# Kernel optimization log

Measured on AMD Instinct MI355X. Metric: run time of the kernel, lower is better.

## Reference

```python
import jax, jax.numpy as jnp
import numpy as np

N, D, H = 4096, 256, 8
NEG = -4294967295.0  # -2**32 + 1, as in masked_fill


def _layernorm(x, g, b, eps=1e-5):
    mu = jnp.mean(x, axis=-1, keepdims=True)
    var = jnp.var(x, axis=-1, keepdims=True)
    return (x - mu) * jax.lax.rsqrt(var + eps) * g + b


def setup_inputs() -> dict:
    key = jax.random.key(0)
    ks = jax.random.split(key, 12)
    s = 0.02
    return {
        "x": jax.random.normal(ks[0], (N, D), jnp.float32),
        "mask_idx": jax.random.randint(ks[1], (N,), 0, 2, jnp.int32),
        "spatial": jax.random.normal(ks[2], (N, N), jnp.float32),
        "edge": jax.random.normal(ks[3], (N, N), jnp.float32),
        "ln1_g": jnp.ones((D,), jnp.float32),
        "ln1_b": jnp.zeros((D,), jnp.float32),
        "Wq": jax.random.normal(ks[4], (H, D, D), jnp.float32) * s,
        "bq": jnp.zeros((H, D), jnp.float32),
        "Wk": jax.random.normal(ks[5], (H, D, D), jnp.float32) * s,
        "bk": jnp.zeros((H, D), jnp.float32),
        "Wv": jax.random.normal(ks[6], (H, D, D), jnp.float32) * s,
        "bv": jnp.zeros((H, D), jnp.float32),
        "Wo": jax.random.normal(ks[7], (D, H * D), jnp.float32) * s,
        "bo": jnp.zeros((D,), jnp.float32),
        "ln2_g": jnp.ones((D,), jnp.float32),
        "ln2_b": jnp.zeros((D,), jnp.float32),
        "Wff": jax.random.normal(ks[8], (D, D), jnp.float32) * s,
        "bff": jnp.zeros((D,), jnp.float32),
    }


def reference(x, mask_idx, spatial, edge, ln1_g, ln1_b, Wq, bq, Wk, bk, Wv, bv,
              Wo, bo, ln2_g, ln2_b, Wff, bff):
    x_ln = _layernorm(x, ln1_g, ln1_b)
    # per-head projections, torch Linear: y = x W^T + b ; q,k,v: [H, N, D]
    q = jnp.einsum('nd,hed->hne', x_ln, Wq) + bq[:, None, :]
    k = jnp.einsum('nd,hed->hne', x_ln, Wk) + bk[:, None, :]
    v = jnp.einsum('nd,hed->hne', x_ln, Wv) + bv[:, None, :]
    scale = 1.0 / jnp.sqrt(jnp.float32(D))  # dim_q ** 0.5
    a = jnp.einsum('hne,hme->hnm', q, k) * scale  # [H, N, N]
    a = a + spatial[None] + edge[None]
    mask0 = (mask_idx[:, None] * mask_idx[None, :]) == 0  # [N, N]
    a = jnp.where(mask0[None], jnp.float32(NEG), a)
    p = jax.nn.softmax(a, axis=-1)
    p = jnp.where(mask0[None], 0.0, p)
    heads = jnp.einsum('hnm,hme->hne', p, v)  # [H, N, D]
    cat = jnp.transpose(heads, (1, 0, 2)).reshape(N, H * D)
    x_out = cat @ Wo.T + bo + x
    x_attn = _layernorm(x_out, ln2_g, ln2_b) @ Wff.T + bff + x_out
    return x_attn
```

## Files before the change

### kernel.cpp

```cpp
#include <hip/hip_runtime.h>
#include <hip/hip_bf16.h>
#include <hip/hip_fp16.h>
#include <string.h>

typedef unsigned short u16;
typedef __attribute__((ext_vector_type(8))) short short8;
typedef __attribute__((ext_vector_type(4))) float floatx4;
typedef __attribute__((ext_vector_type(16))) float floatx16;

#define N_TOK 4096
#define D_DIM 256
#define H_HEAD 8

__device__ __forceinline__ u16 f2b(float f){
  __hip_bfloat16 h = __float2bfloat16(f);
  return *reinterpret_cast<u16*>(&h);
}
__device__ __forceinline__ float b2f(u16 u){
  union { unsigned u; float f; } c; c.u = ((unsigned)u) << 16; return c.f;
}
__device__ __forceinline__ float h2f(u16 u){
  __half h; *reinterpret_cast<u16*>(&h) = u; return __half2float(h);
}
__device__ __forceinline__ u16 f2h(float f){
  __half h = __float2half(f); return *reinterpret_cast<u16*>(&h);
}
__device__ __forceinline__ unsigned pk2bf(float a, float b){
  __hip_bfloat162 h = __float22bfloat162_rn(make_float2(a, b));
  return *reinterpret_cast<unsigned*>(&h);
}

__device__ __forceinline__ void glds16(const void* g, void* l){
  __builtin_amdgcn_global_load_lds(
      (const __attribute__((address_space(1))) unsigned int*)g,
      (__attribute__((address_space(3))) unsigned int*)l, 16, 0, 0);
}

__global__ void fused_prep(const float* __restrict__ Wq, const float* __restrict__ Wk,
                           const float* __restrict__ Wv, const float* __restrict__ Wo,
                           const float* __restrict__ Wff,
                           const float* __restrict__ bq, const float* __restrict__ bk,
                           const float* __restrict__ bv,
                           u16* __restrict__ wqkv, u16* __restrict__ wo_b,
                           u16* __restrict__ wff_b, float* __restrict__ bqkv){
  int bid = blockIdx.x;
  if (bid == 1056){
    int t = threadIdx.x;
    for (int j = 0; j < 24; ++j){
      int idx = t + j*256;
      float v;
      if (idx < 2048) v = bq[idx];
      else if (idx < 4096) v = bk[idx - 2048];
      else v = bv[idx - 4096];
      bqkv[idx] = v;
    }
    return;
  }
  const float* src; u16* dst; int base;
  if      (bid < 256) { src = Wq;  dst = wqkv;            base = bid; }
  else if (bid < 512) { src = Wk;  dst = wqkv + 524288;   base = bid - 256; }
  else if (bid < 768) { src = Wv;  dst = wqkv + 1048576;  base = bid - 512; }
  else if (bid < 1024){ src = Wo;  dst = wo_b;            base = bid - 768; }
  else                { src = Wff; dst = wff_b;           base = bid - 1024; }
  int i = (base*256 + threadIdx.x)*8;
  float4 a = *(const float4*)(src + i);
  float4 b = *(const float4*)(src + i + 4);
  u16 u[8] = {f2b(a.x),f2b(a.y),f2b(a.z),f2b(a.w),f2b(b.x),f2b(b.y),f2b(b.z),f2b(b.w)};
  *(short8*)(dst + i) = *(short8*)u;
}

__global__ void ln_kernel(const float* __restrict__ x, const float* __restrict__ g,
                          const float* __restrict__ b, u16* __restrict__ out){
  const int row = blockIdx.x;
  const int t = threadIdx.x;
  float v = x[(size_t)row*D_DIM + t];
  float s = v, ss = v*v;
  #pragma unroll
  for (int off = 32; off > 0; off >>= 1){
    s  += __shfl_down(s,  off);
    ss += __shfl_down(ss, off);
  }
  __shared__ float ls[4], lss[4];
  const int w = t >> 6, lane = t & 63;
  if (lane == 0){ ls[w] = s; lss[w] = ss; }
  __syncthreads();
  if (t == 0){
    float S  = ls[0]+ls[1]+ls[2]+ls[3];
    float SS = lss[0]+lss[1]+lss[2]+lss[3];
    float mu = S * (1.0f/D_DIM);
    float var = SS * (1.0f/D_DIM) - mu*mu;
    ls[0] = mu; lss[0] = rsqrtf(var + 1e-5f);
  }
  __syncthreads();
  float mu = ls[0], rs = lss[0];
  out[(size_t)row*D_DIM + t] = f2b((v - mu)*rs*g[t] + b[t]);
}

__global__ void ln_sum(const float* __restrict__ p0, const float* __restrict__ p1,
                       const float* __restrict__ bo, const float* __restrict__ x,
                       const float* __restrict__ g, const float* __restrict__ b,
                       float* __restrict__ xout, u16* __restrict__ xln2){
  const int row = blockIdx.x;
  const int t = threadIdx.x;
  const size_t idx = (size_t)row*D_DIM + t;
  float v = p0[idx] + p1[idx] + bo[t] + x[idx];
  float s = v, ss = v*v;
  #pragma unroll
  for (int off = 32; off > 0; off >>= 1){
    s  += __shfl_down(s,  off);
    ss += __shfl_down(ss, off);
  }
  __shared__ float ls[4], lss[4];
  const int w = t >> 6, lane = t & 63;
  if (lane == 0){ ls[w] = s; lss[w] = ss; }
  __syncthreads();
  if (t == 0){
    float S  = ls[0]+ls[1]+ls[2]+ls[3];
    float SS = lss[0]+lss[1]+lss[2]+lss[3];
    float mu = S * (1.0f/D_DIM);
    float var = SS * (1.0f/D_DIM) - mu*mu;
    ls[0] = mu; lss[0] = rsqrtf(var + 1e-5f);
  }
  __syncthreads();
  float mu = ls[0], rs = lss[0];
  xout[idx] = v;
  xln2[idx] = f2b((v - mu)*rs*g[t] + b[t]);
}

__global__ void make_biasW(const float* __restrict__ sp, const float* __restrict__ ed,
                           const int* __restrict__ mask, u16* __restrict__ out){
  __shared__ u16 bh[32][64];
  const int tg = blockIdx.x, q32 = blockIdx.y;
  const int t = threadIdx.x;
  const float L2E = 1.4426950408889634f;
  const u16 NINF = 0xFC00;
  {
    int ql = t>>3, kc = (t&7)*8;
    size_t off = (size_t)(q32*32 + ql)*N_TOK + tg*64 + kc;
    float4 s0 = *(const float4*)(sp + off);
    float4 s1 = *(const float4*)(sp + off + 4);
    float4 e0 = *(const float4*)(ed + off);
    float4 e1 = *(const float4*)(ed + off + 4);
    int mr = mask[q32*32 + ql];
    int4 m0 = *(const int4*)(mask + tg*64 + kc);
    int4 m1 = *(const int4*)(mask + tg*64 + kc + 4);
    bh[ql][kc+0] = (mr*m0.x)==0 ? NINF : f2h((s0.x+e0.x)*L2E);
    bh[ql][kc+1] = (mr*m0.y)==0 ? NINF : f2h((s0.y+e0.y)*L2E);
    bh[ql][kc+2] = (mr*m0.z)==0 ? NINF : f2h((s0.z+e0.z)*L2E);
    bh[ql][kc+3] = (mr*m0.w)==0 ? NINF : f2h((s0.w+e0.w)*L2E);
    bh[ql][kc+4] = (mr*m1.x)==0 ? NINF : f2h((s1.x+e1.x)*L2E);
    bh[ql][kc+5] = (mr*m1.y)==0 ? NINF : f2h((s1.y+e1.y)*L2E);
    bh[ql][kc+6] = (mr*m1.z)==0 ? NINF : f2h((s1.z+e1.z)*L2E);
    bh[ql][kc+7] = (mr*m1.w)==0 ? NINF : f2h((s1.w+e1.w)*L2E);
  }
  __syncthreads();
  int lane2 = t>>2, j0 = (t&3)*8;
  u16 tmp[8];
  #pragma unroll
  for (int jj = 0; jj < 8; ++jj){
    int j = j0 + jj;
    int nb = j>>4, reg = j&15;
    int kvl = nb*32 + (reg&3) + 8*(reg>>2) + 4*(lane2>>5);
    tmp[jj] = bh[lane2&31][kvl];
  }
  u16* dst = out + (((size_t)q32*64 + tg)*64 + lane2)*32 + j0;
  *(short8*)dst = *(short8*)tmp;
}

__global__ void transpose_v(const u16* __restrict__ v, u16* __restrict__ vt){
  __shared__ u16 t[64][72];
  const int h = blockIdx.z;
  const int n0 = blockIdx.x*64, e0 = blockIdx.y*64;
  const int tid = threadIdx.x;
  const int r = tid >> 2;
  const int c = (tid & 3)*16;
  const u16* src = v + ((size_t)h*N_TOK + n0 + r)*D_DIM + e0 + c;
  short8 a = *(const short8*)src;
  short8 b = *(const short8*)(src + 8);
  #pragma unroll
  for (int i = 0; i < 8; ++i){ t[r][c+i] = ((u16*)&a)[i]; t[r][c+8+i] = ((u16*)&b)[i]; }
  __syncthreads();
  u16 tmp[16];
  #pragma unroll
  for (int i = 0; i < 16; ++i) tmp[i] = t[c+i][r];
  u16* dst = vt + ((size_t)h*D_DIM + e0 + r)*N_TOK + n0 + c;
  *(short8*)dst       = *(short8*)tmp;
  *(short8*)(dst + 8) = *(short8*)(tmp + 8);
}

template<int BM, int BN, int MODE>
__launch_bounds__(256, 2)
__global__ void gemm_bt(const u16* __restrict__ A, const u16* __restrict__ B, int K,
                        int lda, int ldb,
                        const float* __restrict__ bias, const float* __restrict__ resid,
                        void* __restrict__ Cout){
  constexpr int BK = 32;
  constexpr int WM = BM/2, WN = BN/2, FM = WM/16, FN = WN/16;
  constexpr int CApW = BM/64;
  constexpr int CBpW = BN/64;
  __shared__ u16 As[BM*BK];
  __shared__ u16 Bs[BN*BK];
  const int tid = threadIdx.x, w = tid>>6, lane = tid&63;
  const int quad = lane>>4, c16 = lane&15;
  const int wr = w>>1, wc = w&1;
  const int rowT = blockIdx.y*BM, colT = blockIdx.x*BN;
  const int lr = lane>>2;
  const int spos = lane&3;
  const int koff = (MODE == 3) ? (int)blockIdx.z*K : 0;

  floatx4 acc[FM][FN] = {};

  for (int k0 = 0; k0 < K; k0 += BK){
    #pragma unroll
    for (int i = 0; i < CApW; ++i){
      int ch = w*CApW + i;
      int row = ch*16 + lr;
      int gch = spos ^ ((row>>1)&3);
      const u16* g = A + (size_t)(rowT + row)*lda + koff + k0 + gch*8;
      glds16(g, As + ch*512);
    }
    #pragma unroll
    for (int i = 0; i < CBpW; ++i){
      int ch = w*CBpW + i;
      int row = ch*16 + lr;
      int gch = spos ^ ((row>>1)&3);
      const u16* g = B + (size_t)(colT + row)*ldb + koff + k0 + gch*8;
      glds16(g, Bs + ch*512);
    }
    __syncthreads();
    short8 af[FM], bf[FN];
    #pragma unroll
    for (int i = 0; i < FM; ++i){
      int row = wr*WM + i*16 + c16;
      int slot = quad ^ ((row>>1)&3);
      af[i] = *(const short8*)&As[row*BK + slot*8];
    }
    #pragma unroll
    for (int j = 0; j < FN; ++j){
      int row = wc*WN + j*16 + c16;
      int slot = quad ^ ((row>>1)&3);
      bf[j] = *(const short8*)&Bs[row*BK + slot*8];
    }
    #pragma unroll
    for (int i = 0; i < FM; ++i)
      #pragma unroll
      for (int j = 0; j < FN; ++j)
        acc[i][j] = __builtin_amdgcn_mfma_f32_16x16x32_bf16(af[i], bf[j], acc[i][j], 0, 0, 0);
    __syncthreads();
  }

  if (MODE == 0){
    u16* o = (u16*)Cout;
    #pragma unroll
    for (int i = 0; i < FM; ++i)
      #pragma unroll
      for (int j = 0; j < FN; ++j){
        int col = colT + wc*WN + j*16 + c16;
        float bv = bias[col];
        float sc = (col < 2048) ? 0.09016994374947424f : 1.0f;
        size_t obase = (size_t)(col>>8)*((size_t)N_TOK*D_DIM) + (col & 255);
        #pragma unroll
        for (int r = 0; r < 4; ++r){
          int row = rowT + wr*WM + i*16 + quad*4 + r;
          o[obase + (size_t)row*D_DIM] = f2b((acc[i][j][r] + bv)*sc);
        }
      }
  } else if (MODE == 2){
    float* o = (float*)Cout;
    #pragma unroll
    for (int i = 0; i < FM; ++i)
      #pragma unroll
      for (int j = 0; j < FN; ++j){
        int col = colT + wc*WN + j*16 + c16;
        float bv = bias[col];
        #pragma unroll
        for (int r = 0; r < 4; ++r){
          int row = rowT + wr*WM + i*16 + quad*4 + r;
          size_t idx = (size_t)row*D_DIM + col;
          o[idx] = acc[i][j][r] + bv + resid[idx];
        }
      }
  } else {
    float* o = (float*)Cout + (size_t)blockIdx.z*((size_t)N_TOK*D_DIM);
    #pragma unroll
    for (int i = 0; i < FM; ++i)
      #pragma unroll
      for (int j = 0; j < FN; ++j){
        int col = colT + wc*WN + j*16 + c16;
        #pragma unroll
        for (int r = 0; r < 4; ++r){
          int row = rowT + wr*WM + i*16 + quad*4 + r;
          o[(size_t)row*D_DIM + col] = acc[i][j][r];
        }
      }
  }
}

__launch_bounds__(512, 2)
__global__ void attn_kernel(const u16* __restrict__ Q, const u16* __restrict__ Kg,
                            const u16* __restrict__ Vt, const u16* __restrict__ biasW,
                            u16* __restrict__ cat0, u16* __restrict__ cat1,
                            float* __restrict__ lsum4){
  extern __shared__ __align__(16) u16 lds[];
  u16* Ks = lds;
  u16* Vs = lds + 16384;
  u16* Ps = lds + 32768;
  const int bid = blockIdx.x;
  const int swz = (bid & 7)*64 + (bid >> 3);
  const int bx = swz & 31, h = (swz >> 5) & 7, spl = swz >> 8;
  const int tid = threadIdx.x, w = tid>>6, lane = tid&63;
  const int hi = lane>>5, l31 = lane&31;
  const int qg = w>>1, kvh = w&1;
  const int qh = w&1, ev = w>>1;
  const int qbase = bx*128;
  const size_t hoff = (size_t)h*N_TOK*D_DIM;
  u16* cs = spl ? cat1 : cat0;

  short8 qf[16];
  {
    const u16* qp = Q + hoff + (size_t)(qbase + qg*32 + l31)*D_DIM + hi*8;
    #pragma unroll
    for (int ks = 0; ks < 16; ++ks) qf[ks] = *(const short8*)(qp + ks*16);
  }

  floatx16 o00 = {}, o01 = {}, o10 = {}, o11 = {};
  float l_lane = 0.f;

  const u16* Kb0 = Kg + hoff + (size_t)spl*2048*D_DIM;
  const u16* Vb0 = Vt + hoff + spl*2048;
  const u16* bWb = biasW + ((((size_t)(bx*4 + qg))*64 + spl*32)*64 + lane)*32 + kvh*16;

  short8 bv0 = *(const short8*)(bWb);
  short8 bv1 = *(const short8*)(bWb + 8);
  {
    #pragma unroll
    for (int i = 0; i < 4; ++i){
      int ch = w*4 + i;
      int row = ch*2 + hi;
      int gch = l31 ^ (row&7);
      glds16(Kb0 + (size_t)row*D_DIM + gch*8, Ks + ch*512);
      int vrow = ch*8 + (lane>>3);
      int vgch = (lane&7) ^ (vrow&7);
      glds16(Vb0 + (size_t)vrow*N_TOK + vgch*8, Vs + ch*512);
    }
  }
  __syncthreads();

  for (int t = 0; t < 32; ++t){
    const int tn = (t + 1) & 31;

    floatx16 sa = {}, sb = {};
    const int krow = kvh*32 + l31;
    __builtin_amdgcn_s_setprio(1);
    #pragma unroll
    for (int ks = 0; ks < 16; ++ks){
      int slot = (2*ks + hi) ^ (l31&7);
      short8 ka = *(const short8*)&Ks[krow*256 + slot*8];
      if (ks & 1) sb = __builtin_amdgcn_mfma_f32_32x32x16_bf16(ka, qf[ks], sb, 0, 0, 0);
      else        sa = __builtin_amdgcn_mfma_f32_32x32x16_bf16(ka, qf[ks], sa, 0, 0, 0);
    }
    __builtin_amdgcn_s_setprio(0);

    {
      const int q = qg*32 + l31;
      #pragma unroll
      for (int g = 0; g < 4; ++g){
        u16 b0 = (g < 2) ? ((u16*)&bv0)[4*g+0] : ((u16*)&bv1)[4*(g-2)+0];
        u16 b1 = (g < 2) ? ((u16*)&bv0)[4*g+1] : ((u16*)&bv1)[4*(g-2)+1];
        u16 b2 = (g < 2) ? ((u16*)&bv0)[4*g+2] : ((u16*)&bv1)[4*(g-2)+2];
        u16 b3 = (g < 2) ? ((u16*)&bv0)[4*g+3] : ((u16*)&bv1)[4*(g-2)+3];
        float p0 = exp2f(sa[4*g+0] + sb[4*g+0] + h2f(b0));
        float p1 = exp2f(sa[4*g+1] + sb[4*g+1] + h2f(b1));
        float p2 = exp2f(sa[4*g+2] + sb[4*g+2] + h2f(b2));
        float p3 = exp2f(sa[4*g+3] + sb[4*g+3] + h2f(b3));
        l_lane += (p0 + p1) + (p2 + p3);
        uint2 pw;
        pw.x = pk2bf(p0, p1);
        pw.y = pk2bf(p2, p3);
        int slot = (kvh*4 + g) ^ (l31&7);
        *(uint2*)&Ps[q*64 + slot*8 + hi*4] = pw;
      }
    }
    __syncthreads();

    {
      const u16* Kb = Kb0 + (size_t)tn*64*D_DIM;
      #pragma unroll
      for (int i = 0; i < 4; ++i){
        int ch = w*4 + i;
        int row = ch*2 + hi;
        int gch = l31 ^ (row&7);
        glds16(Kb + (size_t)row*D_DIM + gch*8, Ks + ch*512);
      }
      const u16* bW = bWb + (size_t)tn*64*32;
      bv0 = *(const short8*)(bW);
      bv1 = *(const short8*)(bW + 8);
    }

    __builtin_amdgcn_s_setprio(1);
    #pragma unroll
    for (int ks2 = 0; ks2 < 4; ++ks2){
      int cA = ks2*2 + hi;
      int sl = cA ^ (l31&7);
      short8 pf0 = *(const short8*)&Ps[(qh*64 +      l31)*64 + sl*8];
      short8 pf1 = *(const short8*)&Ps[(qh*64 + 32 + l31)*64 + sl*8];
      short8 vf0 = *(const short8*)&Vs[(ev*64 +      l31)*64 + sl*8];
      short8 vf1 = *(const short8*)&Vs[(ev*64 + 32 + l31)*64 + sl*8];
      o00 = __builtin_amdgcn_mfma_f32_32x32x16_bf16(pf0, vf0, o00, 0, 0, 0);
      o01 = __builtin_amdgcn_mfma_f32_32x32x16_bf16(pf0, vf1, o01, 0, 0, 0);
      o10 = __builtin_amdgcn_mfma_f32_32x32x16_bf16(pf1, vf0, o10, 0, 0, 0);
      o11 = __builtin_amdgcn_mfma_f32_32x32x16_bf16(pf1, vf1, o11, 0, 0, 0);
    }
    __builtin_amdgcn_s_setprio(0);
    __syncthreads();

    {
      const u16* Vb = Vb0 + tn*64;
      #pragma unroll
      for (int i = 0; i < 4; ++i){
        int ch = w*4 + i;
        int vrow = ch*8 + (lane>>3);
        int vgch = (lane&7) ^ (vrow&7);
        glds16(Vb + (size_t)vrow*N_TOK + vgch*8, Vs + ch*512);
      }
    }
  }

  l_lane += __shfl_xor(l_lane, 32, 64);
  if (hi == 0)
    lsum4[(((size_t)spl*2 + kvh)*H_HEAD + h)*N_TOK + qbase + qg*32 + l31] = l_lane;

  #pragma unroll
  for (int reg = 0; reg < 16; ++reg){
    int qr = (reg&3) + 8*(reg>>2) + 4*hi;
    int q0 = qbase + qh*64 + qr;
    size_t c0 = (size_t)q0*(H_HEAD*D_DIM) + h*D_DIM + ev*64 + l31;
    size_t c1 = (size_t)(q0+32)*(H_HEAD*D_DIM) + h*D_DIM + ev*64 + l31;
    cs[c0]      = f2b(o00[reg]);
    cs[c0 + 32] = f2b(o01[reg]);
    cs[c1]      = f2b(o10[reg]);
    cs[c1 + 32] = f2b(o11[reg]);
  }
}

__global__ void combine2(const u16* __restrict__ c0, const u16* __restrict__ c1,
                         const float* __restrict__ lsum4, u16* __restrict__ cat){
  const int q = blockIdx.x;
  const int t = threadIdx.x;
  const int col = t*8;
  const int h = t >> 5;
  float l = 0.f;
  #pragma unroll
  for (int s = 0; s < 4; ++s)
    l += lsum4[((size_t)s*H_HEAD + h)*N_TOK + q];
  float inv = (l > 0.f) ? 1.0f/l : 0.f;
  size_t base = (size_t)q*(H_HEAD*D_DIM) + col;
  short8 a = *(const short8*)(c0 + base);
  short8 b = *(const short8*)(c1 + base);
  u16 o[8];
  #pragma unroll
  for (int i = 0; i < 8; ++i)
    o[i] = f2b((b2f(((u16*)&a)[i]) + b2f(((u16*)&b)[i]))*inv);
  *(short8*)(cat + base) = *(short8*)o;
}

extern "C" void kernel_launch(void* const* d_in, const int* in_sizes, int n_in,
                              void* d_out, int out_size, void* d_ws, size_t ws_size,
                              hipStream_t stream){
  const float* x    = (const float*)d_in[0];
  const int*   mask = (const int*)  d_in[1];
  const float* sp   = (const float*)d_in[2];
  const float* ed   = (const float*)d_in[3];
  const float* g1   = (const float*)d_in[4];
  const float* b1   = (const float*)d_in[5];
  const float* Wq   = (const float*)d_in[6];
  const float* bq   = (const float*)d_in[7];
  const float* Wk   = (const float*)d_in[8];
  const float* bk   = (const float*)d_in[9];
  const float* Wv   = (const float*)d_in[10];
  const float* bv   = (const float*)d_in[11];
  const float* Wo   = (const float*)d_in[12];
  const float* bo   = (const float*)d_in[13];
  const float* g2   = (const float*)d_in[14];
  const float* b2   = (const float*)d_in[15];
  const float* Wff  = (const float*)d_in[16];
  const float* bff  = (const float*)d_in[17];
  float* out = (float*)d_out;
  char* ws = (char*)d_ws;

  constexpr size_t MB = 1ull<<20;
  u16*   wqkv   = (u16*)  (ws + 0);
  u16*   wo_b   = (u16*)  (ws + 3*MB);
  u16*   wff_b  = (u16*)  (ws + 4*MB);
  float* bqkv   = (float*)(ws + 4*MB + 256*1024);
  u16*   xln    = (u16*)  (ws + 4*MB + 512*1024);
  float* lsum4  = (float*)(ws + 6*MB + 512*1024);
  u16*   qkv    = (u16*)  (ws + 7*MB);
  u16*   vt     = (u16*)  (ws + 55*MB);
  u16*   biasW  = (u16*)  (ws + 71*MB);
  u16*   cat0   = (u16*)  (ws + 39*MB);
  u16*   cat1   = (u16*)  (ws + 103*MB);
  u16*   cat    = (u16*)  (ws + 7*MB);
  float* pK     = (float*)(ws + 23*MB);
  float* xout   = (float*)(ws + 31*MB);
  u16*   xln2   = (u16*)  (ws + 35*MB);
  const size_t TS = (size_t)H_HEAD*N_TOK*D_DIM;

  fused_prep<<<1057, 256, 0, stream>>>(Wq, Wk, Wv, Wo, Wff, bq, bk, bv,
                                       wqkv, wo_b, wff_b, bqkv);
  ln_kernel<<<N_TOK, 256, 0, stream>>>(x, g1, b1, xln);

  gemm_bt<128,128,0><<<dim3(48, 32), 256, 0, stream>>>(xln, wqkv, 256, 256, 256,
                                                       bqkv, nullptr, qkv);

  transpose_v<<<dim3(64, 4, 8), 256, 0, stream>>>(qkv + 2*TS, vt);

  make_biasW<<<dim3(64, 128), 256, 0, stream>>>(sp, ed, mask, biasW);

  hipFuncSetAttribute((const void*)attn_kernel,
                      hipFuncAttributeMaxDynamicSharedMemorySize, 81920);
  attn_kernel<<<dim3(512), 512, 81920, stream>>>(qkv, qkv + TS, vt, biasW,
                                                 cat0, cat1, lsum4);

  combine2<<<N_TOK, 256, 0, stream>>>(cat0, cat1, lsum4, cat);

  gemm_bt<64,64,3><<<dim3(4, 64, 2), 256, 0, stream>>>(cat, wo_b, 1024, 2048, 2048,
                                                       nullptr, nullptr, pK);

  ln_sum<<<N_TOK, 256, 0, stream>>>(pK, pK + (size_t)N_TOK*D_DIM, bo, x, g2, b2,
                                    xout, xln2);

  gemm_bt<64,64,2><<<dim3(4, 64), 256, 0, stream>>>(xln2, wff_b, 256, 256, 256,
                                                    bff, xout, out);
}
```

Before: 455.5 us.

## Double-buffer K and V tiles in attention kernel with vmcnt-based waits

Splits the K and V shared-memory staging into two buffers each, so the next tiles are prefetched while the current ones are consumed. The full __syncthreads calls are replaced with s_waitcnt vmcnt plus s_barrier, and sched_barrier fences keep the asynchronous global-to-LDS copies in order. This targets global load latency on the K/V stream. In exchange, LDS per block grows to 144KB, which likely drops occupancy from two blocks per CU to one, and the hand-counted vmcnt values make the code fragile.

```diff
diff --git a/kernel.cpp b/kernel.cpp
--- a/kernel.cpp
+++ b/kernel.cpp
@@ -302,9 +302,11 @@
                             u16* __restrict__ cat0, u16* __restrict__ cat1,
                             float* __restrict__ lsum4){
   extern __shared__ __align__(16) u16 lds[];
-  u16* Ks = lds;
-  u16* Vs = lds + 16384;
-  u16* Ps = lds + 32768;
+  u16* Ks0 = lds;
+  u16* Ks1 = lds + 16384;
+  u16* Vs0 = lds + 32768;
+  u16* Vs1 = lds + 49152;
+  u16* Ps  = lds + 65536;
   const int bid = blockIdx.x;
   const int swz = (bid & 7)*64 + (bid >> 3);
   const int bx = swz & 31, h = (swz >> 5) & 7, spl = swz >> 8;
@@ -316,38 +318,67 @@
   const size_t hoff = (size_t)h*N_TOK*D_DIM;
   u16* cs = spl ? cat1 : cat0;
 
-  short8 qf[16];
-  {
-    const u16* qp = Q + hoff + (size_t)(qbase + qg*32 + l31)*D_DIM + hi*8;
-    #pragma unroll
-    for (int ks = 0; ks < 16; ++ks) qf[ks] = *(const short8*)(qp + ks*16);
-  }
-
-  floatx16 o00 = {}, o01 = {}, o10 = {}, o11 = {};
-  float l_lane = 0.f;
-
   const u16* Kb0 = Kg + hoff + (size_t)spl*2048*D_DIM;
   const u16* Vb0 = Vt + hoff + spl*2048;
   const u16* bWb = biasW + ((((size_t)(bx*4 + qg))*64 + spl*32)*64 + lane)*32 + kvh*16;
 
-  short8 bv0 = *(const short8*)(bWb);
-  short8 bv1 = *(const short8*)(bWb + 8);
-  {
+  auto stageK = [&](u16* buf, int tile){
+    const u16* Kb = Kb0 + (size_t)tile*64*D_DIM;
     #pragma unroll
     for (int i = 0; i < 4; ++i){
       int ch = w*4 + i;
       int row = ch*2 + hi;
       int gch = l31 ^ (row&7);
-      glds16(Kb0 + (size_t)row*D_DIM + gch*8, Ks + ch*512);
+      glds16(Kb + (size_t)row*D_DIM + gch*8, buf + ch*512);
+    }
+  };
+  auto stageV = [&](u16* buf, int tile){
+    const u16* Vb = Vb0 + tile*64;
+    #pragma unroll
+    for (int i = 0; i < 4; ++i){
+      int ch = w*4 + i;
       int vrow = ch*8 + (lane>>3);
       int vgch = (lane&7) ^ (vrow&7);
-      glds16(Vb0 + (size_t)vrow*N_TOK + vgch*8, Vs + ch*512);
-    }
-  }
-  __syncthreads();
+      glds16(Vb + (size_t)vrow*N_TOK + vgch*8, buf + ch*512);
+    }
+  };
+
+  short8 qf[16];
+  {
+    const u16* qp = Q + hoff + (size_t)(qbase + qg*32 + l31)*D_DIM + hi*8;
+    #pragma unroll
+    for (int ks = 0; ks < 16; ++ks) qf[ks] = *(const short8*)(qp + ks*16);
+  }
+
+  floatx16 o00 = {}, o01 = {}, o10 = {}, o11 = {};
+  float l_lane = 0.f;
+
+  __builtin_amdgcn_sched_barrier(0);
+  stageK(Ks0, 0);
+  __builtin_amdgcn_sched_barrier(0);
+  stageV(Vs0, 0);
+  short8 bv0 = *(const short8*)(bWb);
+  short8 bv1 = *(const short8*)(bWb + 8);
+  __builtin_amdgcn_sched_barrier(0);
+  stageK(Ks1, 1);
+  __builtin_amdgcn_sched_barrier(0);
 
   for (int t = 0; t < 32; ++t){
-    const int tn = (t + 1) & 31;
+    const int tn = (t+1 < 32) ? t+1 : 31;
+    const int t2 = (t+2 < 32) ? t+2 : 31;
+    u16* KsC = (t & 1) ? Ks1 : Ks0;
+    u16* VsC = (t & 1) ? Vs1 : Vs0;
+    u16* VsN = (t & 1) ? Vs0 : Vs1;
+
+    asm volatile("s_waitcnt vmcnt(10)" ::: "memory");
+    __builtin_amdgcn_s_barrier();
+    __builtin_amdgcn_sched_barrier(0);
+
+    stageV(VsN, tn);
+    const u16* bWn = bWb + (size_t)tn*64*32;
+    short8 nbv0 = *(const short8*)(bWn);
+    short8 nbv1 = *(const short8*)(bWn + 8);
+    __builtin_amdgcn_sched_barrier(0);
 
     floatx16 sa = {}, sb = {};
     const int krow = kvh*32 + l31;
@@ -355,7 +386,7 @@
     #pragma unroll
     for (int ks = 0; ks < 16; ++ks){
       int slot = (2*ks + hi) ^ (l31&7);
-      short8 ka = *(const short8*)&Ks[krow*256 + slot*8];
+      short8 ka = *(const short8*)&KsC[krow*256 + slot*8];
       if (ks & 1) sb = __builtin_amdgcn_mfma_f32_32x32x16_bf16(ka, qf[ks], sb, 0, 0, 0);
       else        sa = __builtin_amdgcn_mfma_f32_32x32x16_bf16(ka, qf[ks], sa, 0, 0, 0);
     }
@@ -381,21 +412,10 @@
         *(uint2*)&Ps[q*64 + slot*8 + hi*4] = pw;
       }
     }
-    __syncthreads();
-
-    {
-      const u16* Kb = Kb0 + (size_t)tn*64*D_DIM;
-      #pragma unroll
-      for (int i = 0; i < 4; ++i){
-        int ch = w*4 + i;
-        int row = ch*2 + hi;
-        int gch = l31 ^ (row&7);
-        glds16(Kb + (size_t)row*D_DIM + gch*8, Ks + ch*512);
-      }
-      const u16* bW = bWb + (size_t)tn*64*32;
-      bv0 = *(const short8*)(bW);
-      bv1 = *(const short8*)(bW + 8);
-    }
+
+    asm volatile("s_waitcnt vmcnt(10) lgkmcnt(0)" ::: "memory");
+    __builtin_amdgcn_s_barrier();
+    __builtin_amdgcn_sched_barrier(0);
 
     __builtin_amdgcn_s_setprio(1);
     #pragma unroll
@@ -404,26 +424,20 @@
       int sl = cA ^ (l31&7);
       short8 pf0 = *(const short8*)&Ps[(qh*64 +      l31)*64 + sl*8];
       short8 pf1 = *(const short8*)&Ps[(qh*64 + 32 + l31)*64 + sl*8];
-      short8 vf0 = *(const short8*)&Vs[(ev*64 +      l31)*64 + sl*8];
-      short8 vf1 = *(const short8*)&Vs[(ev*64 + 32 + l31)*64 + sl*8];
+      short8 vf0 = *(const short8*)&VsC[(ev*64 +      l31)*64 + sl*8];
+      short8 vf1 = *(const short8*)&VsC[(ev*64 + 32 + l31)*64 + sl*8];
       o00 = __builtin_amdgcn_mfma_f32_32x32x16_bf16(pf0, vf0, o00, 0, 0, 0);
       o01 = __builtin_amdgcn_mfma_f32_32x32x16_bf16(pf0, vf1, o01, 0, 0, 0);
       o10 = __builtin_amdgcn_mfma_f32_32x32x16_bf16(pf1, vf0, o10, 0, 0, 0);
       o11 = __builtin_amdgcn_mfma_f32_32x32x16_bf16(pf1, vf1, o11, 0, 0, 0);
     }
     __builtin_amdgcn_s_setprio(0);
-    __syncthreads();
-
-    {
-      const u16* Vb = Vb0 + tn*64;
-      #pragma unroll
-      for (int i = 0; i < 4; ++i){
-        int ch = w*4 + i;
-        int vrow = ch*8 + (lane>>3);
-        int vgch = (lane&7) ^ (vrow&7);
-        glds16(Vb + (size_t)vrow*N_TOK + vgch*8, Vs + ch*512);
-      }
-    }
+    __builtin_amdgcn_sched_barrier(0);
+
+    stageK(KsC, t2);
+    __builtin_amdgcn_sched_barrier(0);
+
+    bv0 = nbv0; bv1 = nbv1;
   }
 
   l_lane += __shfl_xor(l_lane, 32, 64);
@@ -518,9 +532,9 @@
   make_biasW<<<dim3(64, 128), 256, 0, stream>>>(sp, ed, mask, biasW);
 
   hipFuncSetAttribute((const void*)attn_kernel,
-                      hipFuncAttributeMaxDynamicSharedMemorySize, 81920);
-  attn_kernel<<<dim3(512), 512, 81920, stream>>>(qkv, qkv + TS, vt, biasW,
-                                                 cat0, cat1, lsum4);
+                      hipFuncAttributeMaxDynamicSharedMemorySize, 147456);
+  attn_kernel<<<dim3(512), 512, 147456, stream>>>(qkv, qkv + TS, vt, biasW,
+                                                  cat0, cat1, lsum4);
 
   combine2<<<N_TOK, 256, 0, stream>>>(cat0, cat1, lsum4, cat);
 
```

Measured after the change: 452.2 us. About the same (-0.7%).
